# Kernel tuning notes

Measured on AMD Instinct MI355X. Metric: run time of the kernel, lower is better.

## Reference

```python
import jax, jax.numpy as jnp
import numpy as np
import itertools


def _shift(x, di, dj):
    """y[..., i, j] = x[..., i+di, j+dj]; out-of-bounds filled with dtype min."""
    neg = jnp.finfo(x.dtype).min
    H, W = x.shape[-2], x.shape[-1]
    if di != 0:
        d = min(abs(di), H)
        pad = jnp.full(x.shape[:-2] + (d, W), neg, x.dtype)
        x = jnp.concatenate([x[..., d:, :], pad], -2) if di > 0 else jnp.concatenate([pad, x[..., :H - d, :]], -2)
    if dj != 0:
        d = min(abs(dj), W)
        pad = jnp.full(x.shape[:-1] + (d,), neg, x.dtype)
        x = jnp.concatenate([x[..., d:], pad], -1) if dj > 0 else jnp.concatenate([pad, x[..., :W - d]], -1)
    return x


def _dir_cummax(x, di, dj):
    """out[i,j] = max_{k>=0} x[i+k*di, j+k*dj], computed in O(log n) doubling steps."""
    H, W = x.shape[-2], x.shape[-1]
    n = max(H * (di != 0), W * (dj != 0), 1)
    s = 1
    while s < n:
        x = jnp.maximum(x, _shift(x, di * s, dj * s))
        s *= 2
    return x


# TP, BP, LP, RP, PD, PAD, ND, NAD (directional cumulative-max pools)
_DIRS = [(1, 0), (-1, 0), (0, 1), (0, -1), (1, 1), (1, -1), (-1, -1), (-1, 1)]


def _subset_weights():
    # Mean over all 255 non-empty subsets of the subset-mean of member pools
    # collapses to a fixed per-pool weight (== 1/8 each by binomial symmetry).
    subsets = [s for L in range(1, 9) for s in itertools.combinations(range(8), L)]
    w = np.zeros(8, np.float64)
    for s in subsets:
        for i in s:
            w[i] += 1.0 / len(s)
    w /= len(subsets)
    return jnp.asarray(w, jnp.float32)


def setup_inputs() -> dict:
    key = jax.random.key(0)
    x = jax.random.normal(key, (8, 256, 128, 128), jnp.float32)
    return {"x": x}


def reference(x):
    pools = jnp.stack([_dir_cummax(x, di, dj) for di, dj in _DIRS])  # [8,B,C,H,W]
    w = _subset_weights().astype(x.dtype)
    return jnp.einsum('p,pbchw->bchw', w, pools)
```

## Files before the change

kernel.cpp:

```cpp
#include <hip/hip_runtime.h>


#define NPIX 16384
#define NEGF (-3.402823466e38f)

typedef __fp16 half2v __attribute__((ext_vector_type(2)));

template <int CTRL>
__device__ __forceinline__ float dpp_movf(float oldv, float src) {
  return __int_as_float(__builtin_amdgcn_update_dpp(
      __float_as_int(oldv), __float_as_int(src), CTRL, 0xf, 0xf, false));
}
#define WAVE_SHR1 0x138
#define WAVE_SHL1 0x130

#define DPP_MAXSTEP(y, ctrl, rmask)                                          \
  y = fmaxf(y, __int_as_float(__builtin_amdgcn_update_dpp(                   \
                 __float_as_int(y), __float_as_int(y), ctrl, rmask, 0xf,     \
                 false)))

template <bool MIR>
__device__ __forceinline__ void run(const float* __restrict__ xim,
                                    float* __restrict__ oim,
                                    unsigned* __restrict__ part, const int l) {
  const int off = MIR ? (63 - l) * 2 : l * 2;
  const int slot = MIR ? (63 - l) : l;

  float v0 = NEGF, v1 = NEGF, d0 = NEGF, d1 = NEGF, a0 = NEGF, a1 = NEGF;

  float2 G[4];
#pragma unroll
  for (int k = 0; k < 4; ++k) {
    const int row = MIR ? 127 - k : k;
    G[k] = *(const float2*)(xim + (row << 7) + off);
  }

  for (int tb = 0; tb < 64; tb += 4) {
#pragma unroll
    for (int k = 0; k < 4; ++k) {
      const int t = tb + k;
      const float2 xv = G[k];
      const int pr = t + 4;
      const int prow = MIR ? 127 - pr : pr;
      G[k] = *(const float2*)(xim + (prow << 7) + off);

      const float x0 = MIR ? xv.y : xv.x;
      const float x1 = MIR ? xv.x : xv.y;

      v0 = fmaxf(v0, x0);
      v1 = fmaxf(v1, x1);

      const float pd = dpp_movf<WAVE_SHR1>(NEGF, d1);
      const float nd0 = fmaxf(x0, pd);
      const float nd1 = fmaxf(x1, d0);
      d0 = nd0; d1 = nd1;

      const float pa = dpp_movf<WAVE_SHL1>(NEGF, a0);
      const float na1 = fmaxf(x1, pa);
      const float na0 = fmaxf(x0, a1);
      a0 = na0; a1 = na1;

      float y = fmaxf(x0, x1);
      DPP_MAXSTEP(y, 0x111, 0xf);
      DPP_MAXSTEP(y, 0x112, 0xf);
      DPP_MAXSTEP(y, 0x114, 0xf);
      DPP_MAXSTEP(y, 0x118, 0xf);
      DPP_MAXSTEP(y, 0x142, 0xa);
      DPP_MAXSTEP(y, 0x143, 0xc);
      const float ex = dpp_movf<WAVE_SHR1>(NEGF, y);
      const float s0 = fmaxf(ex, x0);

      const float p0 = (v0 + d0) + (a0 + s0);
      const float p1 = (v1 + d1) + (a1 + y);

      const int row = MIR ? 127 - t : t;
      const half2v h = MIR ? __builtin_amdgcn_cvt_pkrtz(p1, p0)
                           : __builtin_amdgcn_cvt_pkrtz(p0, p1);
      part[(row << 6) + slot] = __builtin_bit_cast(unsigned, h);
    }
  }

  __syncthreads();

  {
    const int row64 = MIR ? 63 : 64;
    unsigned pb = part[(row64 << 6) + slot];
    for (int tb = 64; tb < 128; tb += 4) {
#pragma unroll
      for (int k = 0; k < 4; ++k) {
        const int t = tb + k;
        const float2 xv = G[k];
        const int pr = (t + 4 < 128) ? t + 4 : 127;
        const int prow = MIR ? 127 - pr : pr;
        G[k] = *(const float2*)(xim + (prow << 7) + off);

        const unsigned q = pb;
        const int tn = (t + 1 < 128) ? t + 1 : 127;
        const int nrow = MIR ? 127 - tn : tn;
        pb = part[(nrow << 6) + slot];

        const float x0 = MIR ? xv.y : xv.x;
        const float x1 = MIR ? xv.x : xv.y;

        v0 = fmaxf(v0, x0);
        v1 = fmaxf(v1, x1);

        const float pd = dpp_movf<WAVE_SHR1>(NEGF, d1);
        const float nd0 = fmaxf(x0, pd);
        const float nd1 = fmaxf(x1, d0);
        d0 = nd0; d1 = nd1;

        const float pa = dpp_movf<WAVE_SHL1>(NEGF, a0);
        const float na1 = fmaxf(x1, pa);
        const float na0 = fmaxf(x0, a1);
        a0 = na0; a1 = na1;

        float y = fmaxf(x0, x1);
        DPP_MAXSTEP(y, 0x111, 0xf);
        DPP_MAXSTEP(y, 0x112, 0xf);
        DPP_MAXSTEP(y, 0x114, 0xf);
        DPP_MAXSTEP(y, 0x118, 0xf);
        DPP_MAXSTEP(y, 0x142, 0xa);
        DPP_MAXSTEP(y, 0x143, 0xc);
        const float ex = dpp_movf<WAVE_SHR1>(NEGF, y);
        const float s0 = fmaxf(ex, x0);

        const float p0 = (v0 + d0) + (a0 + s0);
        const float p1 = (v1 + d1) + (a1 + y);

        const half2v hq = __builtin_bit_cast(half2v, q);
        const float q0 = (float)(MIR ? hq.y : hq.x);
        const float q1 = (float)(MIR ? hq.x : hq.y);
        const float o0 = (p0 + q0) * 0.125f;
        const float o1 = (p1 + q1) * 0.125f;

        const int row = MIR ? 127 - t : t;
        const float2 ov = MIR ? make_float2(o1, o0) : make_float2(o0, o1);
        *(float2*)(oim + (row << 7) + off) = ov;
      }
    }
  }
}

__global__ __launch_bounds__(128) void pool255_sweep(
    const float* __restrict__ x, float* __restrict__ out) {
  __shared__ unsigned part[NPIX / 2];
  const int img = blockIdx.x;
  const float* __restrict__ xim = x + (size_t)img * NPIX;
  float* __restrict__ oim = out + (size_t)img * NPIX;
  const int l = threadIdx.x & 63;

  if (threadIdx.x < 64)
    run<false>(xim, oim, part, l);
  else
    run<true>(xim, oim, part, l);
}

extern "C" void kernel_launch(void* const* d_in, const int* in_sizes, int n_in,
                              void* d_out, int out_size, void* d_ws,
                              size_t ws_size, hipStream_t stream) {
  const float* x = (const float*)d_in[0];
  float* out = (float*)d_out;
  const int n_img = in_sizes[0] / NPIX;
  pool255_sweep<<<n_img, 128, 0, stream>>>(x, out);
}
```

Measured before the change: 75.51 us.

## Deepen prefetch to eight rows, persistent grid, nontemporal stores, lighter barrier

Doubles the software prefetch depth for input rows from four to eight and prefetches eight LDS partial rows ahead instead of one. Output stores become nontemporal, the block barrier becomes a raw waitcnt plus s_barrier, and the launch is capped at 1024 blocks that loop over images grid-stride. The intent is to hide more global-load latency and cut per-block launch overhead. The cost is higher register pressure and fewer resident blocks than images, which may reduce the parallelism available to hide latency.

```diff
diff --git a/kernel.cpp b/kernel.cpp
--- a/kernel.cpp
+++ b/kernel.cpp
@@ -19,6 +19,10 @@
                  __float_as_int(y), __float_as_int(y), ctrl, rmask, 0xf,     \
                  false)))
 
+__device__ __forceinline__ void lds_barrier() {
+  asm volatile("s_waitcnt lgkmcnt(0)\n\ts_barrier" ::: "memory");
+}
+
 template <bool MIR>
 __device__ __forceinline__ void run(const float* __restrict__ xim,
                                     float* __restrict__ oim,
@@ -28,19 +32,19 @@
 
   float v0 = NEGF, v1 = NEGF, d0 = NEGF, d1 = NEGF, a0 = NEGF, a1 = NEGF;
 
-  float2 G[4];
+  float2 G[8];
 #pragma unroll
-  for (int k = 0; k < 4; ++k) {
+  for (int k = 0; k < 8; ++k) {
     const int row = MIR ? 127 - k : k;
     G[k] = *(const float2*)(xim + (row << 7) + off);
   }
 
-  for (int tb = 0; tb < 64; tb += 4) {
+  for (int tb = 0; tb < 64; tb += 8) {
 #pragma unroll
-    for (int k = 0; k < 4; ++k) {
+    for (int k = 0; k < 8; ++k) {
       const int t = tb + k;
       const float2 xv = G[k];
-      const int pr = t + 4;
+      const int pr = t + 8;
       const int prow = MIR ? 127 - pr : pr;
       G[k] = *(const float2*)(xim + (prow << 7) + off);
 
@@ -80,24 +84,26 @@
     }
   }
 
-  __syncthreads();
+  lds_barrier();
 
   {
-    const int row64 = MIR ? 63 : 64;
-    unsigned pb = part[(row64 << 6) + slot];
-    for (int tb = 64; tb < 128; tb += 4) {
+    unsigned Q[8];
 #pragma unroll
-      for (int k = 0; k < 4; ++k) {
+    for (int k = 0; k < 8; ++k) {
+      const int row = MIR ? 127 - (64 + k) : (64 + k);
+      Q[k] = part[(row << 6) + slot];
+    }
+    for (int tb = 64; tb < 128; tb += 8) {
+#pragma unroll
+      for (int k = 0; k < 8; ++k) {
         const int t = tb + k;
         const float2 xv = G[k];
-        const int pr = (t + 4 < 128) ? t + 4 : 127;
+        const int pr = (t + 8 < 128) ? t + 8 : 127;
         const int prow = MIR ? 127 - pr : pr;
         G[k] = *(const float2*)(xim + (prow << 7) + off);
 
-        const unsigned q = pb;
-        const int tn = (t + 1 < 128) ? t + 1 : 127;
-        const int nrow = MIR ? 127 - tn : tn;
-        pb = part[(nrow << 6) + slot];
+        const unsigned q = Q[k];
+        Q[k] = part[(prow << 6) + slot];
 
         const float x0 = MIR ? xv.y : xv.x;
         const float x1 = MIR ? xv.x : xv.y;
@@ -136,24 +142,27 @@
 
         const int row = MIR ? 127 - t : t;
         const float2 ov = MIR ? make_float2(o1, o0) : make_float2(o0, o1);
-        *(float2*)(oim + (row << 7) + off) = ov;
+        __builtin_nontemporal_store(
+            __builtin_bit_cast(unsigned long long, ov),
+            (unsigned long long*)(oim + (row << 7) + off));
       }
     }
   }
 }
 
 __global__ __launch_bounds__(128) void pool255_sweep(
-    const float* __restrict__ x, float* __restrict__ out) {
+    const float* __restrict__ x, float* __restrict__ out, int n_img) {
   __shared__ unsigned part[NPIX / 2];
-  const int img = blockIdx.x;
-  const float* __restrict__ xim = x + (size_t)img * NPIX;
-  float* __restrict__ oim = out + (size_t)img * NPIX;
   const int l = threadIdx.x & 63;
-
-  if (threadIdx.x < 64)
-    run<false>(xim, oim, part, l);
-  else
-    run<true>(xim, oim, part, l);
+  for (int img = blockIdx.x; img < n_img; img += gridDim.x) {
+    const float* __restrict__ xim = x + (size_t)img * NPIX;
+    float* __restrict__ oim = out + (size_t)img * NPIX;
+    if (threadIdx.x < 64)
+      run<false>(xim, oim, part, l);
+    else
+      run<true>(xim, oim, part, l);
+    lds_barrier();
+  }
 }
 
 extern "C" void kernel_launch(void* const* d_in, const int* in_sizes, int n_in,
@@ -162,5 +171,6 @@
   const float* x = (const float*)d_in[0];
   float* out = (float*)d_out;
   const int n_img = in_sizes[0] / NPIX;
-  pool255_sweep<<<n_img, 128, 0, stream>>>(x, out);
+  const int grid = (n_img < 1024) ? n_img : 1024;
+  pool255_sweep<<<grid, 128, 0, stream>>>(x, out, n_img);
 }
```

Measured after the change: 63.53 us. 1.19x faster.
